# Kernel tuning notes

Hardware: AMD Instinct MI355X
Metric: run time of the kernel (lower is better)

The kernel has to match this reference:

```python
import jax, jax.numpy as jnp
import numpy as np

B, NQ, NK, D = 64, 1024, 1024, 128
MASK_VALUE = -1e6


def setup_inputs() -> dict:
    key = jax.random.key(0)
    kq, kk, kv, kl = jax.random.split(key, 4)
    queries = jax.random.normal(kq, (B, NQ, D), dtype=jnp.float32)
    keys = jax.random.normal(kk, (B, NK, D), dtype=jnp.float32)
    values = jax.random.normal(kv, (B, NK, D), dtype=jnp.float32)
    valid_lens = jax.random.randint(kl, (B,), 1, NK + 1, dtype=jnp.int32)
    return {"queries": queries, "keys": keys, "values": values, "valid_lens": valid_lens}


def reference(queries, keys, values, valid_lens):
    d = queries.shape[-1]
    # scores: [B, Nq, Nk]
    scores = jnp.einsum("bqd,bkd->bqk", queries, keys) / jnp.sqrt(jnp.float32(d))
    # valid_lens [B] -> mask over last (key) axis, same for every query row
    key_pos = jnp.arange(scores.shape[-1])  # [Nk]
    mask = key_pos[None, None, :] < valid_lens[:, None, None]  # [B,1,Nk] broadcast
    scores = jnp.where(mask, scores, jnp.float32(MASK_VALUE))
    attn = jax.nn.softmax(scores, axis=-1)
    # dropout p=0.0 (eval): identity
    return jnp.einsum("bqk,bkd->bqd", attn, values)
```

## Files before the change

### kernel.cpp

```cpp
#include <hip/hip_runtime.h>

typedef __bf16 bf16x8 __attribute__((ext_vector_type(8)));
typedef __bf16 bf16x2 __attribute__((ext_vector_type(2)));
typedef float f32x4 __attribute__((ext_vector_type(4)));
typedef int i32x4 __attribute__((ext_vector_type(4)));

namespace {
constexpr int kNQ = 1024;
constexpr int kNK = 1024;
constexpr int kD = 128;
constexpr int kBK = 32;
constexpr int kTileElems = 4096;
constexpr float kScaleLog2e = 0.12751742f;
}

__device__ __forceinline__ int packbf(float a, float b) {
    bf16x2 t; t[0] = (__bf16)a; t[1] = (__bf16)b;
    return __builtin_bit_cast(int, t);
}

__device__ __forceinline__ void async16(const __bf16* g, const __bf16* l) {
    __builtin_amdgcn_global_load_lds(
        (const __attribute__((address_space(1))) void*)g,
        (__attribute__((address_space(3))) void*)l, 16, 0, 0);
}

__global__ void repack(const float* __restrict__ K, const float* __restrict__ V,
                       const int* __restrict__ VL,
                       __bf16* __restrict__ Kimg, __bf16* __restrict__ Vimg,
                       int* __restrict__ perm) {
    const int blk = blockIdx.x;

    if (blk == 64 * 32) {
        const int t = threadIdx.x;
        if (t < 64) {
            const int v = VL[t];
            int rank = 0;
            for (int j = 0; j < 64; ++j) {
                const int vj = VL[j];
                rank += (vj > v) || (vj == v && j < t);
            }
            perm[rank] = t;
        }
        return;
    }

    const int b = blk >> 5, t = blk & 31;
    if (t * kBK >= VL[b]) return;
    const int tid = threadIdx.x;
    __shared__ float vbuf[32 * 132];

    const size_t tileofs = (size_t)(b * 32 + t) * kTileElems;

    #pragma unroll
    for (int it = 0; it < 2; ++it) {
        const int chunk = tid + it * 256;
        const int k = chunk >> 4;
        const int p = chunk & 15;
        const int c = p ^ (k & 15);
        const float* src = K + (((size_t)b * kNK + t * kBK + k) * kD + c * 8);
        const f32x4 x0 = *(const f32x4*)src;
        const f32x4 x1 = *(const f32x4*)(src + 4);
        bf16x8 h;
        #pragma unroll
        for (int j = 0; j < 4; ++j) { h[j] = (__bf16)x0[j]; h[4 + j] = (__bf16)x1[j]; }
        *(bf16x8*)(Kimg + tileofs + chunk * 8) = h;
    }

    {
        const int r = tid >> 3, col0 = (tid & 7) * 16;
        const float* src = V + (((size_t)b * kNK + t * kBK + r) * kD + col0);
        #pragma unroll
        for (int j = 0; j < 4; ++j) {
            const f32x4 x = *(const f32x4*)(src + j * 4);
            *(f32x4*)&vbuf[r * 132 + col0 + j * 4] = x;
        }
    }
    __syncthreads();
    #pragma unroll
    for (int it = 0; it < 2; ++it) {
        const int chunk = tid + it * 256;
        const int d = chunk >> 2;
        const int p = chunk & 3;
        const int q = p ^ ((d >> 1) & 3);
        bf16x8 h;
        #pragma unroll
        for (int j = 0; j < 8; ++j) h[j] = (__bf16)vbuf[(q * 8 + j) * 132 + d];
        *(bf16x8*)(Vimg + tileofs + chunk * 8) = h;
    }
}

__global__ __launch_bounds__(512, 4)
void fa_fwd(const float* __restrict__ Q, const int* __restrict__ VL,
            const int* __restrict__ perm, const __bf16* __restrict__ Kimg,
            const __bf16* __restrict__ Vimg, float* __restrict__ O)
{
    __shared__ __align__(16) __bf16 kls[4][kTileElems];
    __shared__ __align__(16) __bf16 vls[4][kTileElems];

    const int tid  = threadIdx.x;
    const int wave = tid >> 6;
    const int lane = tid & 63;
    const int quad = lane >> 4;
    const int c16  = lane & 15;

    const int i = blockIdx.x;
    const int j = i & 255;
    const int rank = (i >> 8) ? (511 - j) : j;

    const int b  = perm[rank >> 3];
    const int q0 = (rank & 7) * 128 + wave * 16;

    const int valid  = VL[b];
    const int ntiles = (valid + kBK - 1) / kBK;
    const size_t bT  = (size_t)b * 32;

    auto stage = [&](int slot, int t) {
        const __bf16* kg = Kimg + (bT + t) * kTileElems;
        const __bf16* vg = Vimg + (bT + t) * kTileElems;
        const int seg = wave * 512;
        async16(kg + seg + lane * 8, &kls[slot][seg]);
        async16(vg + seg + lane * 8, &vls[slot][seg]);
    };

    stage(0, 0);
    if (ntiles > 1) stage(1, 1);

    bf16x8 qf[4];
    {
        const float* qp = Q + ((size_t)b * kNQ + q0 + c16) * kD + quad * 8;
        #pragma unroll
        for (int f = 0; f < 4; ++f) {
            const f32x4 x0 = *(const f32x4*)(qp + f * 32);
            const f32x4 x1 = *(const f32x4*)(qp + f * 32 + 4);
            #pragma unroll
            for (int jj = 0; jj < 4; ++jj) {
                qf[f][jj]     = (__bf16)x0[jj];
                qf[f][4 + jj] = (__bf16)x1[jj];
            }
        }
    }

    bf16x8 ones;
    #pragma unroll
    for (int jj = 0; jj < 8; ++jj) ones[jj] = (__bf16)1.0f;

    f32x4 acc[9];
    #pragma unroll
    for (int f = 0; f < 9; ++f) {
        acc[f][0] = 0.f; acc[f][1] = 0.f; acc[f][2] = 0.f; acc[f][3] = 0.f;
    }

    const int a0 = ((quad & 1) << 7) + (c16 << 2);
    const int a1 = a0 + 64;
    const bool lo = quad < 2;

    const int vsw = (quad ^ ((c16 >> 1) & 3)) << 3;

    for (int t = 0; t < ntiles; ++t) {
        if (t + 2 < ntiles) {
            stage((t + 2) & 3, t + 2);
            asm volatile("s_waitcnt vmcnt(4)" ::: "memory");
        } else if (t + 1 < ntiles) {
            asm volatile("s_waitcnt vmcnt(2)" ::: "memory");
        } else {
            asm volatile("s_waitcnt vmcnt(0)" ::: "memory");
        }
        __builtin_amdgcn_s_barrier();
        __builtin_amdgcn_sched_barrier(0);

        const __bf16* kbuf = kls[t & 3];
        const __bf16* vbuf = vls[t & 3];

        f32x4 s0a = {0.f,0.f,0.f,0.f}, s0b = {0.f,0.f,0.f,0.f};
        f32x4 s1a = {0.f,0.f,0.f,0.f}, s1b = {0.f,0.f,0.f,0.f};
        __builtin_amdgcn_s_setprio(1);
        #pragma unroll
        for (int f = 0; f < 2; ++f) {
            const bf16x8 kf = *(const bf16x8*)&kbuf[c16 * 128 + (((f * 4 + quad) ^ c16) << 3)];
            s0a = __builtin_amdgcn_mfma_f32_16x16x32_bf16(kf, qf[f], s0a, 0, 0, 0);
        }
        #pragma unroll
        for (int f = 2; f < 4; ++f) {
            const bf16x8 kf = *(const bf16x8*)&kbuf[c16 * 128 + (((f * 4 + quad) ^ c16) << 3)];
            s0b = __builtin_amdgcn_mfma_f32_16x16x32_bf16(kf, qf[f], s0b, 0, 0, 0);
        }
        #pragma unroll
        for (int f = 0; f < 2; ++f) {
            const bf16x8 kf = *(const bf16x8*)&kbuf[(16 + c16) * 128 + (((f * 4 + quad) ^ c16) << 3)];
            s1a = __builtin_amdgcn_mfma_f32_16x16x32_bf16(kf, qf[f], s1a, 0, 0, 0);
        }
        #pragma unroll
        for (int f = 2; f < 4; ++f) {
            const bf16x8 kf = *(const bf16x8*)&kbuf[(16 + c16) * 128 + (((f * 4 + quad) ^ c16) << 3)];
            s1b = __builtin_amdgcn_mfma_f32_16x16x32_bf16(kf, qf[f], s1b, 0, 0, 0);
        }
        __builtin_amdgcn_s_setprio(0);
        f32x4 s0 = s0a + s0b;
        f32x4 s1 = s1a + s1b;

        const int kb = t * kBK;
        if (kb + kBK > valid) {
            #pragma unroll
            for (int r = 0; r < 4; ++r) {
                if (kb + quad * 4 + r >= valid)      s0[r] = -1e30f;
                if (kb + 16 + quad * 4 + r >= valid) s1[r] = -1e30f;
            }
        }

        #pragma unroll
        for (int r = 0; r < 4; ++r) {
            s0[r] = __builtin_amdgcn_exp2f(s0[r] * kScaleLog2e);
            s1[r] = __builtin_amdgcn_exp2f(s1[r] * kScaleLog2e);
        }

        const int pp01 = packbf(s0[0], s0[1]), pp23 = packbf(s0[2], s0[3]);
        const int qq01 = packbf(s1[0], s1[1]), qq23 = packbf(s1[2], s1[3]);
        const int b0p = __builtin_amdgcn_ds_bpermute(a0, pp01);
        const int b0q = __builtin_amdgcn_ds_bpermute(a0, qq01);
        const int b1p = __builtin_amdgcn_ds_bpermute(a0, pp23);
        const int b1q = __builtin_amdgcn_ds_bpermute(a0, qq23);
        const int b2p = __builtin_amdgcn_ds_bpermute(a1, pp01);
        const int b2q = __builtin_amdgcn_ds_bpermute(a1, qq01);
        const int b3p = __builtin_amdgcn_ds_bpermute(a1, pp23);
        const int b3q = __builtin_amdgcn_ds_bpermute(a1, qq23);
        i32x4 pd;
        pd[0] = lo ? b0p : b0q;
        pd[1] = lo ? b1p : b1q;
        pd[2] = lo ? b2p : b2q;
        pd[3] = lo ? b3p : b3q;
        const bf16x8 pf = __builtin_bit_cast(bf16x8, pd);

        __builtin_amdgcn_s_setprio(1);
        acc[8] = __builtin_amdgcn_mfma_f32_16x16x32_bf16(pf, ones, acc[8], 0, 0, 0);
        #pragma unroll
        for (int f = 0; f < 8; ++f) {
            const bf16x8 vf = *(const bf16x8*)&vbuf[(f * 16 + c16) * 32 + vsw];
            acc[f] = __builtin_amdgcn_mfma_f32_16x16x32_bf16(pf, vf, acc[f], 0, 0, 0);
        }
        __builtin_amdgcn_s_setprio(0);
    }

    float* ob = O + ((size_t)b * kNQ + q0) * kD;
    #pragma unroll
    for (int r = 0; r < 4; ++r) {
        const float inv = 1.0f / acc[8][r];
        #pragma unroll
        for (int f = 0; f < 8; ++f) {
            ob[(quad * 4 + r) * kD + f * 16 + c16] = acc[f][r] * inv;
        }
    }
}

extern "C" void kernel_launch(void* const* d_in, const int* in_sizes, int n_in,
                              void* d_out, int out_size, void* d_ws, size_t ws_size,
                              hipStream_t stream) {
    const float* Q = (const float*)d_in[0];
    const float* K = (const float*)d_in[1];
    const float* V = (const float*)d_in[2];
    const int*  VL = (const int*)d_in[3];
    float* O = (float*)d_out;

    int* perm = (int*)d_ws;
    __bf16* Kimg = (__bf16*)((char*)d_ws + 4096);
    __bf16* Vimg = (__bf16*)((char*)d_ws + 4096 + (size_t)16 * 1024 * 1024);

    repack<<<dim3(64 * 32 + 1), 256, 0, stream>>>(K, V, VL, Kimg, Vimg, perm);
    fa_fwd<<<dim3(512), 512, 0, stream>>>(Q, VL, perm, Kimg, Vimg, O);
}
```

Measured before the change: 164.1 us.

## Process two 16-row query tiles per wave with 256-thread blocks

Each wave now handles 32 query rows as two 16-row sub-tiles that share every K and V fragment read from LDS. This halves the LDS traffic per MFMA and halves the waves per block (256 threads), with each wave issuing twice as many async loads per stage. The cost is more registers per wave (two accumulator sets and two Q fragment sets), with the launch bounds changed to match, and fewer waves available to hide latency.

```diff
diff --git a/kernel.cpp b/kernel.cpp
--- a/kernel.cpp
+++ b/kernel.cpp
@@ -90,7 +90,7 @@
     }
 }
 
-__global__ __launch_bounds__(512, 4)
+__global__ __launch_bounds__(256, 2)
 void fa_fwd(const float* __restrict__ Q, const int* __restrict__ VL,
             const int* __restrict__ perm, const __bf16* __restrict__ Kimg,
             const __bf16* __restrict__ Vimg, float* __restrict__ O)
@@ -109,7 +109,7 @@
     const int rank = (i >> 8) ? (511 - j) : j;
 
     const int b  = perm[rank >> 3];
-    const int q0 = (rank & 7) * 128 + wave * 16;
+    const int q0 = (rank & 7) * 128 + wave * 32;
 
     const int valid  = VL[b];
     const int ntiles = (valid + kBK - 1) / kBK;
@@ -118,25 +118,33 @@
     auto stage = [&](int slot, int t) {
         const __bf16* kg = Kimg + (bT + t) * kTileElems;
         const __bf16* vg = Vimg + (bT + t) * kTileElems;
-        const int seg = wave * 512;
-        async16(kg + seg + lane * 8, &kls[slot][seg]);
-        async16(vg + seg + lane * 8, &vls[slot][seg]);
+        #pragma unroll
+        for (int ii = 0; ii < 2; ++ii) {
+            const int seg = wave * 1024 + ii * 512;
+            async16(kg + seg + lane * 8, &kls[slot][seg]);
+            async16(vg + seg + lane * 8, &vls[slot][seg]);
+        }
     };
 
     stage(0, 0);
     if (ntiles > 1) stage(1, 1);
 
-    bf16x8 qf[4];
+    bf16x8 qfA[4], qfB[4];
     {
-        const float* qp = Q + ((size_t)b * kNQ + q0 + c16) * kD + quad * 8;
+        const float* qpA = Q + ((size_t)b * kNQ + q0 + c16) * kD + quad * 8;
+        const float* qpB = qpA + 16 * kD;
         #pragma unroll
         for (int f = 0; f < 4; ++f) {
-            const f32x4 x0 = *(const f32x4*)(qp + f * 32);
-            const f32x4 x1 = *(const f32x4*)(qp + f * 32 + 4);
+            const f32x4 a0v = *(const f32x4*)(qpA + f * 32);
+            const f32x4 a1v = *(const f32x4*)(qpA + f * 32 + 4);
+            const f32x4 b0v = *(const f32x4*)(qpB + f * 32);
+            const f32x4 b1v = *(const f32x4*)(qpB + f * 32 + 4);
             #pragma unroll
             for (int jj = 0; jj < 4; ++jj) {
-                qf[f][jj]     = (__bf16)x0[jj];
-                qf[f][4 + jj] = (__bf16)x1[jj];
+                qfA[f][jj]     = (__bf16)a0v[jj];
+                qfA[f][4 + jj] = (__bf16)a1v[jj];
+                qfB[f][jj]     = (__bf16)b0v[jj];
+                qfB[f][4 + jj] = (__bf16)b1v[jj];
             }
         }
     }
@@ -145,11 +153,14 @@
     #pragma unroll
     for (int jj = 0; jj < 8; ++jj) ones[jj] = (__bf16)1.0f;
 
-    f32x4 acc[9];
-    #pragma unroll
-    for (int f = 0; f < 9; ++f) {
-        acc[f][0] = 0.f; acc[f][1] = 0.f; acc[f][2] = 0.f; acc[f][3] = 0.f;
-    }
+    f32x4 accA[8], accB[8], lA, lB;
+    #pragma unroll
+    for (int f = 0; f < 8; ++f) {
+        accA[f][0]=0.f; accA[f][1]=0.f; accA[f][2]=0.f; accA[f][3]=0.f;
+        accB[f][0]=0.f; accB[f][1]=0.f; accB[f][2]=0.f; accB[f][3]=0.f;
+    }
+    lA[0]=lA[1]=lA[2]=lA[3]=0.f;
+    lB[0]=lB[1]=lB[2]=lB[3]=0.f;
 
     const int a0 = ((quad & 1) << 7) + (c16 << 2);
     const int a1 = a0 + 64;
@@ -160,9 +171,9 @@
     for (int t = 0; t < ntiles; ++t) {
         if (t + 2 < ntiles) {
             stage((t + 2) & 3, t + 2);
+            asm volatile("s_waitcnt vmcnt(8)" ::: "memory");
+        } else if (t + 1 < ntiles) {
             asm volatile("s_waitcnt vmcnt(4)" ::: "memory");
-        } else if (t + 1 < ntiles) {
-            asm volatile("s_waitcnt vmcnt(2)" ::: "memory");
         } else {
             asm volatile("s_waitcnt vmcnt(0)" ::: "memory");
         }
@@ -172,71 +183,84 @@
         const __bf16* kbuf = kls[t & 3];
         const __bf16* vbuf = vls[t & 3];
 
-        f32x4 s0a = {0.f,0.f,0.f,0.f}, s0b = {0.f,0.f,0.f,0.f};
-        f32x4 s1a = {0.f,0.f,0.f,0.f}, s1b = {0.f,0.f,0.f,0.f};
+        f32x4 sA0 = {0.f,0.f,0.f,0.f}, sA1 = {0.f,0.f,0.f,0.f};
+        f32x4 sB0 = {0.f,0.f,0.f,0.f}, sB1 = {0.f,0.f,0.f,0.f};
         __builtin_amdgcn_s_setprio(1);
         #pragma unroll
-        for (int f = 0; f < 2; ++f) {
-            const bf16x8 kf = *(const bf16x8*)&kbuf[c16 * 128 + (((f * 4 + quad) ^ c16) << 3)];
-            s0a = __builtin_amdgcn_mfma_f32_16x16x32_bf16(kf, qf[f], s0a, 0, 0, 0);
-        }
-        #pragma unroll
-        for (int f = 2; f < 4; ++f) {
-            const bf16x8 kf = *(const bf16x8*)&kbuf[c16 * 128 + (((f * 4 + quad) ^ c16) << 3)];
-            s0b = __builtin_amdgcn_mfma_f32_16x16x32_bf16(kf, qf[f], s0b, 0, 0, 0);
-        }
-        #pragma unroll
-        for (int f = 0; f < 2; ++f) {
-            const bf16x8 kf = *(const bf16x8*)&kbuf[(16 + c16) * 128 + (((f * 4 + quad) ^ c16) << 3)];
-            s1a = __builtin_amdgcn_mfma_f32_16x16x32_bf16(kf, qf[f], s1a, 0, 0, 0);
-        }
-        #pragma unroll
-        for (int f = 2; f < 4; ++f) {
-            const bf16x8 kf = *(const bf16x8*)&kbuf[(16 + c16) * 128 + (((f * 4 + quad) ^ c16) << 3)];
-            s1b = __builtin_amdgcn_mfma_f32_16x16x32_bf16(kf, qf[f], s1b, 0, 0, 0);
+        for (int f = 0; f < 4; ++f) {
+            const int sw = ((f * 4 + quad) ^ c16) << 3;
+            const bf16x8 kf0 = *(const bf16x8*)&kbuf[c16 * 128 + sw];
+            const bf16x8 kf1 = *(const bf16x8*)&kbuf[(16 + c16) * 128 + sw];
+            sA0 = __builtin_amdgcn_mfma_f32_16x16x32_bf16(kf0, qfA[f], sA0, 0, 0, 0);
+            sB0 = __builtin_amdgcn_mfma_f32_16x16x32_bf16(kf0, qfB[f], sB0, 0, 0, 0);
+            sA1 = __builtin_amdgcn_mfma_f32_16x16x32_bf16(kf1, qfA[f], sA1, 0, 0, 0);
+            sB1 = __builtin_amdgcn_mfma_f32_16x16x32_bf16(kf1, qfB[f], sB1, 0, 0, 0);
         }
         __builtin_amdgcn_s_setprio(0);
-        f32x4 s0 = s0a + s0b;
-        f32x4 s1 = s1a + s1b;
 
         const int kb = t * kBK;
         if (kb + kBK > valid) {
             #pragma unroll
             for (int r = 0; r < 4; ++r) {
-                if (kb + quad * 4 + r >= valid)      s0[r] = -1e30f;
-                if (kb + 16 + quad * 4 + r >= valid) s1[r] = -1e30f;
+                if (kb + quad * 4 + r >= valid) { sA0[r] = -1e30f; sB0[r] = -1e30f; }
+                if (kb + 16 + quad * 4 + r >= valid) { sA1[r] = -1e30f; sB1[r] = -1e30f; }
             }
         }
 
         #pragma unroll
         for (int r = 0; r < 4; ++r) {
-            s0[r] = __builtin_amdgcn_exp2f(s0[r] * kScaleLog2e);
-            s1[r] = __builtin_amdgcn_exp2f(s1[r] * kScaleLog2e);
-        }
-
-        const int pp01 = packbf(s0[0], s0[1]), pp23 = packbf(s0[2], s0[3]);
-        const int qq01 = packbf(s1[0], s1[1]), qq23 = packbf(s1[2], s1[3]);
-        const int b0p = __builtin_amdgcn_ds_bpermute(a0, pp01);
-        const int b0q = __builtin_amdgcn_ds_bpermute(a0, qq01);
-        const int b1p = __builtin_amdgcn_ds_bpermute(a0, pp23);
-        const int b1q = __builtin_amdgcn_ds_bpermute(a0, qq23);
-        const int b2p = __builtin_amdgcn_ds_bpermute(a1, pp01);
-        const int b2q = __builtin_amdgcn_ds_bpermute(a1, qq01);
-        const int b3p = __builtin_amdgcn_ds_bpermute(a1, pp23);
-        const int b3q = __builtin_amdgcn_ds_bpermute(a1, qq23);
-        i32x4 pd;
-        pd[0] = lo ? b0p : b0q;
-        pd[1] = lo ? b1p : b1q;
-        pd[2] = lo ? b2p : b2q;
-        pd[3] = lo ? b3p : b3q;
-        const bf16x8 pf = __builtin_bit_cast(bf16x8, pd);
+            sA0[r] = __builtin_amdgcn_exp2f(sA0[r] * kScaleLog2e);
+            sA1[r] = __builtin_amdgcn_exp2f(sA1[r] * kScaleLog2e);
+            sB0[r] = __builtin_amdgcn_exp2f(sB0[r] * kScaleLog2e);
+            sB1[r] = __builtin_amdgcn_exp2f(sB1[r] * kScaleLog2e);
+        }
+
+        bf16x8 pfA, pfB;
+        {
+            const int pp01 = packbf(sA0[0], sA0[1]), pp23 = packbf(sA0[2], sA0[3]);
+            const int qq01 = packbf(sA1[0], sA1[1]), qq23 = packbf(sA1[2], sA1[3]);
+            const int b0p = __builtin_amdgcn_ds_bpermute(a0, pp01);
+            const int b0q = __builtin_amdgcn_ds_bpermute(a0, qq01);
+            const int b1p = __builtin_amdgcn_ds_bpermute(a0, pp23);
+            const int b1q = __builtin_amdgcn_ds_bpermute(a0, qq23);
+            const int b2p = __builtin_amdgcn_ds_bpermute(a1, pp01);
+            const int b2q = __builtin_amdgcn_ds_bpermute(a1, qq01);
+            const int b3p = __builtin_amdgcn_ds_bpermute(a1, pp23);
+            const int b3q = __builtin_amdgcn_ds_bpermute(a1, qq23);
+            i32x4 pd;
+            pd[0] = lo ? b0p : b0q;
+            pd[1] = lo ? b1p : b1q;
+            pd[2] = lo ? b2p : b2q;
+            pd[3] = lo ? b3p : b3q;
+            pfA = __builtin_bit_cast(bf16x8, pd);
+        }
+        {
+            const int pp01 = packbf(sB0[0], sB0[1]), pp23 = packbf(sB0[2], sB0[3]);
+            const int qq01 = packbf(sB1[0], sB1[1]), qq23 = packbf(sB1[2], sB1[3]);
+            const int b0p = __builtin_amdgcn_ds_bpermute(a0, pp01);
+            const int b0q = __builtin_amdgcn_ds_bpermute(a0, qq01);
+            const int b1p = __builtin_amdgcn_ds_bpermute(a0, pp23);
+            const int b1q = __builtin_amdgcn_ds_bpermute(a0, qq23);
+            const int b2p = __builtin_amdgcn_ds_bpermute(a1, pp01);
+            const int b2q = __builtin_amdgcn_ds_bpermute(a1, qq01);
+            const int b3p = __builtin_amdgcn_ds_bpermute(a1, pp23);
+            const int b3q = __builtin_amdgcn_ds_bpermute(a1, qq23);
+            i32x4 pd;
+            pd[0] = lo ? b0p : b0q;
+            pd[1] = lo ? b1p : b1q;
+            pd[2] = lo ? b2p : b2q;
+            pd[3] = lo ? b3p : b3q;
+            pfB = __builtin_bit_cast(bf16x8, pd);
+        }
 
         __builtin_amdgcn_s_setprio(1);
-        acc[8] = __builtin_amdgcn_mfma_f32_16x16x32_bf16(pf, ones, acc[8], 0, 0, 0);
+        lA = __builtin_amdgcn_mfma_f32_16x16x32_bf16(pfA, ones, lA, 0, 0, 0);
+        lB = __builtin_amdgcn_mfma_f32_16x16x32_bf16(pfB, ones, lB, 0, 0, 0);
         #pragma unroll
         for (int f = 0; f < 8; ++f) {
             const bf16x8 vf = *(const bf16x8*)&vbuf[(f * 16 + c16) * 32 + vsw];
-            acc[f] = __builtin_amdgcn_mfma_f32_16x16x32_bf16(pf, vf, acc[f], 0, 0, 0);
+            accA[f] = __builtin_amdgcn_mfma_f32_16x16x32_bf16(pfA, vf, accA[f], 0, 0, 0);
+            accB[f] = __builtin_amdgcn_mfma_f32_16x16x32_bf16(pfB, vf, accB[f], 0, 0, 0);
         }
         __builtin_amdgcn_s_setprio(0);
     }
@@ -244,10 +268,12 @@
     float* ob = O + ((size_t)b * kNQ + q0) * kD;
     #pragma unroll
     for (int r = 0; r < 4; ++r) {
-        const float inv = 1.0f / acc[8][r];
+        const float invA = 1.0f / lA[r];
+        const float invB = 1.0f / lB[r];
         #pragma unroll
         for (int f = 0; f < 8; ++f) {
-            ob[(quad * 4 + r) * kD + f * 16 + c16] = acc[f][r] * inv;
+            ob[(quad * 4 + r) * kD + f * 16 + c16]        = accA[f][r] * invA;
+            ob[(16 + quad * 4 + r) * kD + f * 16 + c16]   = accB[f][r] * invB;
         }
     }
 }
@@ -266,5 +292,5 @@
     __bf16* Vimg = (__bf16*)((char*)d_ws + 4096 + (size_t)16 * 1024 * 1024);
 
     repack<<<dim3(64 * 32 + 1), 256, 0, stream>>>(K, V, VL, Kimg, Vimg, perm);
-    fa_fwd<<<dim3(512), 512, 0, stream>>>(Q, VL, perm, Kimg, Vimg, O);
-}
+    fa_fwd<<<dim3(512), 256, 0, stream>>>(Q, VL, perm, Kimg, Vimg, O);
+}
```

After: 167.9 us. 2.3% more time.

## Process two K/V tiles per loop iteration with a single barrier

Applied to the files above, without the earlier changes.

Restructures the attention main loop so each iteration waits for all outstanding loads, issues one barrier, prefetches the next two tiles, and then runs both QK^T products before both softmax/PV phases. The aim is to halve barrier and wait overhead and to give the scheduler two independent MFMA chains to interleave. The cost is a full vmcnt(0) wait in place of the finer-grained partial waits, which may expose more load latency, plus higher register pressure from holding two tiles of scores at once.

```diff
diff --git a/kernel.cpp b/kernel.cpp
--- a/kernel.cpp
+++ b/kernel.cpp
@@ -157,21 +157,7 @@
 
     const int vsw = (quad ^ ((c16 >> 1) & 3)) << 3;
 
-    for (int t = 0; t < ntiles; ++t) {
-        if (t + 2 < ntiles) {
-            stage((t + 2) & 3, t + 2);
-            asm volatile("s_waitcnt vmcnt(4)" ::: "memory");
-        } else if (t + 1 < ntiles) {
-            asm volatile("s_waitcnt vmcnt(2)" ::: "memory");
-        } else {
-            asm volatile("s_waitcnt vmcnt(0)" ::: "memory");
-        }
-        __builtin_amdgcn_s_barrier();
-        __builtin_amdgcn_sched_barrier(0);
-
-        const __bf16* kbuf = kls[t & 3];
-        const __bf16* vbuf = vls[t & 3];
-
+    auto qk = [&](const __bf16* kbuf, f32x4& s0, f32x4& s1) {
         f32x4 s0a = {0.f,0.f,0.f,0.f}, s0b = {0.f,0.f,0.f,0.f};
         f32x4 s1a = {0.f,0.f,0.f,0.f}, s1b = {0.f,0.f,0.f,0.f};
         __builtin_amdgcn_s_setprio(1);
@@ -196,10 +182,11 @@
             s1b = __builtin_amdgcn_mfma_f32_16x16x32_bf16(kf, qf[f], s1b, 0, 0, 0);
         }
         __builtin_amdgcn_s_setprio(0);
-        f32x4 s0 = s0a + s0b;
-        f32x4 s1 = s1a + s1b;
-
-        const int kb = t * kBK;
+        s0 = s0a + s0b;
+        s1 = s1a + s1b;
+    };
+
+    auto smpv = [&](f32x4 s0, f32x4 s1, const __bf16* vbuf, int kb) {
         if (kb + kBK > valid) {
             #pragma unroll
             for (int r = 0; r < 4; ++r) {
@@ -207,13 +194,11 @@
                 if (kb + 16 + quad * 4 + r >= valid) s1[r] = -1e30f;
             }
         }
-
         #pragma unroll
         for (int r = 0; r < 4; ++r) {
             s0[r] = __builtin_amdgcn_exp2f(s0[r] * kScaleLog2e);
             s1[r] = __builtin_amdgcn_exp2f(s1[r] * kScaleLog2e);
         }
-
         const int pp01 = packbf(s0[0], s0[1]), pp23 = packbf(s0[2], s0[3]);
         const int qq01 = packbf(s1[0], s1[1]), qq23 = packbf(s1[2], s1[3]);
         const int b0p = __builtin_amdgcn_ds_bpermute(a0, pp01);
@@ -239,6 +224,31 @@
             acc[f] = __builtin_amdgcn_mfma_f32_16x16x32_bf16(pf, vf, acc[f], 0, 0, 0);
         }
         __builtin_amdgcn_s_setprio(0);
+    };
+
+    int t = 0;
+    while (t + 1 < ntiles) {
+        asm volatile("s_waitcnt vmcnt(0)" ::: "memory");
+        __builtin_amdgcn_s_barrier();
+        __builtin_amdgcn_sched_barrier(0);
+
+        if (t + 2 < ntiles) stage((t + 2) & 3, t + 2);
+        if (t + 3 < ntiles) stage((t + 3) & 3, t + 3);
+
+        f32x4 s0_0, s1_0, s0_1, s1_1;
+        qk(kls[t & 3], s0_0, s1_0);
+        qk(kls[(t + 1) & 3], s0_1, s1_1);
+        smpv(s0_0, s1_0, vls[t & 3], t * kBK);
+        smpv(s0_1, s1_1, vls[(t + 1) & 3], (t + 1) * kBK);
+        t += 2;
+    }
+    if (t < ntiles) {
+        asm volatile("s_waitcnt vmcnt(0)" ::: "memory");
+        __builtin_amdgcn_s_barrier();
+        __builtin_amdgcn_sched_barrier(0);
+        f32x4 s0_0, s1_0;
+        qk(kls[t & 3], s0_0, s1_0);
+        smpv(s0_0, s1_0, vls[t & 3], t * kBK);
     }
 
     float* ob = O + ((size_t)b * kNQ + q0) * kD;
```

After: 164.4 us. About the same (+0.1%).

## Switch attention kernel to 32x32x16 MFMA with 4 waves of 32 query rows

Applied to the files above, without the earlier changes.

Rewrites the flash-attention inner loop to use 32x32x16 bf16 MFMA instead of 16x16x32. Each wave now handles 32 query rows and the block shrinks to 256 threads. The row-sum is accumulated on the VALU instead of through an extra MFMA against a ones vector. The P operand is rearranged with a cross-half bpermute exchange, and the staging loop issues twice as many async loads per wave. The aim is to raise MFMA efficiency and cut the LDS reads of K and V per query row, at the cost of larger accumulator register footprint and fewer waves per block.

```diff
diff --git a/kernel.cpp b/kernel.cpp
--- a/kernel.cpp
+++ b/kernel.cpp
@@ -3,6 +3,7 @@
 typedef __bf16 bf16x8 __attribute__((ext_vector_type(8)));
 typedef __bf16 bf16x2 __attribute__((ext_vector_type(2)));
 typedef float f32x4 __attribute__((ext_vector_type(4)));
+typedef float f32x16 __attribute__((ext_vector_type(16)));
 typedef int i32x4 __attribute__((ext_vector_type(4)));
 
 namespace {
@@ -90,7 +91,7 @@
     }
 }
 
-__global__ __launch_bounds__(512, 4)
+__global__ __launch_bounds__(256, 2)
 void fa_fwd(const float* __restrict__ Q, const int* __restrict__ VL,
             const int* __restrict__ perm, const __bf16* __restrict__ Kimg,
             const __bf16* __restrict__ Vimg, float* __restrict__ O)
@@ -101,15 +102,15 @@
     const int tid  = threadIdx.x;
     const int wave = tid >> 6;
     const int lane = tid & 63;
-    const int quad = lane >> 4;
-    const int c16  = lane & 15;
+    const int key  = lane & 31;
+    const int hi   = lane >> 5;
 
     const int i = blockIdx.x;
     const int j = i & 255;
     const int rank = (i >> 8) ? (511 - j) : j;
 
     const int b  = perm[rank >> 3];
-    const int q0 = (rank & 7) * 128 + wave * 16;
+    const int q0 = (rank & 7) * 128 + wave * 32;
 
     const int valid  = VL[b];
     const int ntiles = (valid + kBK - 1) / kBK;
@@ -118,51 +119,48 @@
     auto stage = [&](int slot, int t) {
         const __bf16* kg = Kimg + (bT + t) * kTileElems;
         const __bf16* vg = Vimg + (bT + t) * kTileElems;
-        const int seg = wave * 512;
-        async16(kg + seg + lane * 8, &kls[slot][seg]);
-        async16(vg + seg + lane * 8, &vls[slot][seg]);
+        #pragma unroll
+        for (int ii = 0; ii < 2; ++ii) {
+            const int seg = wave * 1024 + ii * 512;
+            async16(kg + seg + lane * 8, &kls[slot][seg]);
+            async16(vg + seg + lane * 8, &vls[slot][seg]);
+        }
     };
 
     stage(0, 0);
     if (ntiles > 1) stage(1, 1);
 
-    bf16x8 qf[4];
+    bf16x8 qf[8];
     {
-        const float* qp = Q + ((size_t)b * kNQ + q0 + c16) * kD + quad * 8;
-        #pragma unroll
-        for (int f = 0; f < 4; ++f) {
-            const f32x4 x0 = *(const f32x4*)(qp + f * 32);
-            const f32x4 x1 = *(const f32x4*)(qp + f * 32 + 4);
+        const float* qp = Q + ((size_t)b * kNQ + q0 + key) * kD + hi * 8;
+        #pragma unroll
+        for (int s = 0; s < 8; ++s) {
+            const f32x4 x0 = *(const f32x4*)(qp + s * 16);
+            const f32x4 x1 = *(const f32x4*)(qp + s * 16 + 4);
             #pragma unroll
             for (int jj = 0; jj < 4; ++jj) {
-                qf[f][jj]     = (__bf16)x0[jj];
-                qf[f][4 + jj] = (__bf16)x1[jj];
+                qf[s][jj]     = (__bf16)x0[jj];
+                qf[s][4 + jj] = (__bf16)x1[jj];
             }
         }
     }
 
-    bf16x8 ones;
-    #pragma unroll
-    for (int jj = 0; jj < 8; ++jj) ones[jj] = (__bf16)1.0f;
-
-    f32x4 acc[9];
-    #pragma unroll
-    for (int f = 0; f < 9; ++f) {
-        acc[f][0] = 0.f; acc[f][1] = 0.f; acc[f][2] = 0.f; acc[f][3] = 0.f;
-    }
-
-    const int a0 = ((quad & 1) << 7) + (c16 << 2);
-    const int a1 = a0 + 64;
-    const bool lo = quad < 2;
-
-    const int vsw = (quad ^ ((c16 >> 1) & 3)) << 3;
+    f32x16 acc0, acc1, acc2, acc3;
+    #pragma unroll
+    for (int r = 0; r < 16; ++r) { acc0[r]=0.f; acc1[r]=0.f; acc2[r]=0.f; acc3[r]=0.f; }
+    float lsum = 0.f;
+
+    const int kterm = key & 15;
+    const int vterm = (key >> 1) & 3;
+    const int xaddr = (lane ^ 32) << 2;
+    const int hi4   = hi << 2;
 
     for (int t = 0; t < ntiles; ++t) {
         if (t + 2 < ntiles) {
             stage((t + 2) & 3, t + 2);
+            asm volatile("s_waitcnt vmcnt(8)" ::: "memory");
+        } else if (t + 1 < ntiles) {
             asm volatile("s_waitcnt vmcnt(4)" ::: "memory");
-        } else if (t + 1 < ntiles) {
-            asm volatile("s_waitcnt vmcnt(2)" ::: "memory");
         } else {
             asm volatile("s_waitcnt vmcnt(0)" ::: "memory");
         }
@@ -172,83 +170,98 @@
         const __bf16* kbuf = kls[t & 3];
         const __bf16* vbuf = vls[t & 3];
 
-        f32x4 s0a = {0.f,0.f,0.f,0.f}, s0b = {0.f,0.f,0.f,0.f};
-        f32x4 s1a = {0.f,0.f,0.f,0.f}, s1b = {0.f,0.f,0.f,0.f};
+        f32x16 sa, sb;
+        #pragma unroll
+        for (int r = 0; r < 16; ++r) { sa[r] = 0.f; sb[r] = 0.f; }
         __builtin_amdgcn_s_setprio(1);
         #pragma unroll
-        for (int f = 0; f < 2; ++f) {
-            const bf16x8 kf = *(const bf16x8*)&kbuf[c16 * 128 + (((f * 4 + quad) ^ c16) << 3)];
-            s0a = __builtin_amdgcn_mfma_f32_16x16x32_bf16(kf, qf[f], s0a, 0, 0, 0);
-        }
-        #pragma unroll
-        for (int f = 2; f < 4; ++f) {
-            const bf16x8 kf = *(const bf16x8*)&kbuf[c16 * 128 + (((f * 4 + quad) ^ c16) << 3)];
-            s0b = __builtin_amdgcn_mfma_f32_16x16x32_bf16(kf, qf[f], s0b, 0, 0, 0);
-        }
-        #pragma unroll
-        for (int f = 0; f < 2; ++f) {
-            const bf16x8 kf = *(const bf16x8*)&kbuf[(16 + c16) * 128 + (((f * 4 + quad) ^ c16) << 3)];
-            s1a = __builtin_amdgcn_mfma_f32_16x16x32_bf16(kf, qf[f], s1a, 0, 0, 0);
-        }
-        #pragma unroll
-        for (int f = 2; f < 4; ++f) {
-            const bf16x8 kf = *(const bf16x8*)&kbuf[(16 + c16) * 128 + (((f * 4 + quad) ^ c16) << 3)];
-            s1b = __builtin_amdgcn_mfma_f32_16x16x32_bf16(kf, qf[f], s1b, 0, 0, 0);
+        for (int s = 0; s < 4; ++s) {
+            const bf16x8 kf = *(const bf16x8*)&kbuf[key * 128 + (((s * 2 + hi) ^ kterm) << 3)];
+            sa = __builtin_amdgcn_mfma_f32_32x32x16_bf16(kf, qf[s], sa, 0, 0, 0);
+        }
+        #pragma unroll
+        for (int s = 4; s < 8; ++s) {
+            const bf16x8 kf = *(const bf16x8*)&kbuf[key * 128 + (((s * 2 + hi) ^ kterm) << 3)];
+            sb = __builtin_amdgcn_mfma_f32_32x32x16_bf16(kf, qf[s], sb, 0, 0, 0);
         }
         __builtin_amdgcn_s_setprio(0);
-        f32x4 s0 = s0a + s0b;
-        f32x4 s1 = s1a + s1b;
+        f32x16 sv = sa + sb;
 
         const int kb = t * kBK;
         if (kb + kBK > valid) {
             #pragma unroll
-            for (int r = 0; r < 4; ++r) {
-                if (kb + quad * 4 + r >= valid)      s0[r] = -1e30f;
-                if (kb + 16 + quad * 4 + r >= valid) s1[r] = -1e30f;
+            for (int r = 0; r < 16; ++r) {
+                const int cr = (r & 3) + 8 * (r >> 2);
+                if (kb + cr + hi4 >= valid) sv[r] = -1e30f;
             }
         }
 
         #pragma unroll
-        for (int r = 0; r < 4; ++r) {
-            s0[r] = __builtin_amdgcn_exp2f(s0[r] * kScaleLog2e);
-            s1[r] = __builtin_amdgcn_exp2f(s1[r] * kScaleLog2e);
-        }
-
-        const int pp01 = packbf(s0[0], s0[1]), pp23 = packbf(s0[2], s0[3]);
-        const int qq01 = packbf(s1[0], s1[1]), qq23 = packbf(s1[2], s1[3]);
-        const int b0p = __builtin_amdgcn_ds_bpermute(a0, pp01);
-        const int b0q = __builtin_amdgcn_ds_bpermute(a0, qq01);
-        const int b1p = __builtin_amdgcn_ds_bpermute(a0, pp23);
-        const int b1q = __builtin_amdgcn_ds_bpermute(a0, qq23);
-        const int b2p = __builtin_amdgcn_ds_bpermute(a1, pp01);
-        const int b2q = __builtin_amdgcn_ds_bpermute(a1, qq01);
-        const int b3p = __builtin_amdgcn_ds_bpermute(a1, pp23);
-        const int b3q = __builtin_amdgcn_ds_bpermute(a1, qq23);
-        i32x4 pd;
-        pd[0] = lo ? b0p : b0q;
-        pd[1] = lo ? b1p : b1q;
-        pd[2] = lo ? b2p : b2q;
-        pd[3] = lo ? b3p : b3q;
-        const bf16x8 pf = __builtin_bit_cast(bf16x8, pd);
+        for (int r = 0; r < 16; ++r) sv[r] = __builtin_amdgcn_exp2f(sv[r] * kScaleLog2e);
+
+        {
+            float a0 = sv[0]+sv[1], a1 = sv[2]+sv[3], a2 = sv[4]+sv[5], a3 = sv[6]+sv[7];
+            float a4 = sv[8]+sv[9], a5 = sv[10]+sv[11], a6 = sv[12]+sv[13], a7 = sv[14]+sv[15];
+            lsum += ((a0+a1)+(a2+a3)) + ((a4+a5)+(a6+a7));
+        }
+
+        int w[8], pw[8];
+        #pragma unroll
+        for (int jp = 0; jp < 8; ++jp) w[jp] = packbf(sv[2*jp], sv[2*jp+1]);
+        #pragma unroll
+        for (int jp = 0; jp < 8; ++jp) pw[jp] = __builtin_amdgcn_ds_bpermute(xaddr, w[jp]);
+
+        i32x4 f0, f1;
+        f0[0] = hi ? pw[2] : w[0];
+        f0[1] = hi ? pw[3] : w[1];
+        f0[2] = hi ? w[2]  : pw[0];
+        f0[3] = hi ? w[3]  : pw[1];
+        f1[0] = hi ? pw[6] : w[4];
+        f1[1] = hi ? pw[7] : w[5];
+        f1[2] = hi ? w[6]  : pw[4];
+        f1[3] = hi ? w[7]  : pw[5];
+        const bf16x8 pfs0 = __builtin_bit_cast(bf16x8, f0);
+        const bf16x8 pfs1 = __builtin_bit_cast(bf16x8, f1);
 
         __builtin_amdgcn_s_setprio(1);
-        acc[8] = __builtin_amdgcn_mfma_f32_16x16x32_bf16(pf, ones, acc[8], 0, 0, 0);
-        #pragma unroll
-        for (int f = 0; f < 8; ++f) {
-            const bf16x8 vf = *(const bf16x8*)&vbuf[(f * 16 + c16) * 32 + vsw];
-            acc[f] = __builtin_amdgcn_mfma_f32_16x16x32_bf16(pf, vf, acc[f], 0, 0, 0);
+        {
+            const int vb0 = key * 32 + (((0 + hi) ^ vterm) << 3);
+            const int vb1 = key * 32 + (((2 + hi) ^ vterm) << 3);
+            const bf16x8 v00 = *(const bf16x8*)&vbuf[0 * 1024 + vb0];
+            const bf16x8 v10 = *(const bf16x8*)&vbuf[1 * 1024 + vb0];
+            const bf16x8 v20 = *(const bf16x8*)&vbuf[2 * 1024 + vb0];
+            const bf16x8 v30 = *(const bf16x8*)&vbuf[3 * 1024 + vb0];
+            acc0 = __builtin_amdgcn_mfma_f32_32x32x16_bf16(pfs0, v00, acc0, 0, 0, 0);
+            acc1 = __builtin_amdgcn_mfma_f32_32x32x16_bf16(pfs0, v10, acc1, 0, 0, 0);
+            acc2 = __builtin_amdgcn_mfma_f32_32x32x16_bf16(pfs0, v20, acc2, 0, 0, 0);
+            acc3 = __builtin_amdgcn_mfma_f32_32x32x16_bf16(pfs0, v30, acc3, 0, 0, 0);
+            const bf16x8 v01 = *(const bf16x8*)&vbuf[0 * 1024 + vb1];
+            const bf16x8 v11 = *(const bf16x8*)&vbuf[1 * 1024 + vb1];
+            const bf16x8 v21 = *(const bf16x8*)&vbuf[2 * 1024 + vb1];
+            const bf16x8 v31 = *(const bf16x8*)&vbuf[3 * 1024 + vb1];
+            acc0 = __builtin_amdgcn_mfma_f32_32x32x16_bf16(pfs1, v01, acc0, 0, 0, 0);
+            acc1 = __builtin_amdgcn_mfma_f32_32x32x16_bf16(pfs1, v11, acc1, 0, 0, 0);
+            acc2 = __builtin_amdgcn_mfma_f32_32x32x16_bf16(pfs1, v21, acc2, 0, 0, 0);
+            acc3 = __builtin_amdgcn_mfma_f32_32x32x16_bf16(pfs1, v31, acc3, 0, 0, 0);
         }
         __builtin_amdgcn_s_setprio(0);
     }
 
+    const int plb = __builtin_amdgcn_ds_bpermute(xaddr, __builtin_bit_cast(int, lsum));
+    const float linv = 1.0f / (lsum + __builtin_bit_cast(float, plb));
     float* ob = O + ((size_t)b * kNQ + q0) * kD;
-    #pragma unroll
-    for (int r = 0; r < 4; ++r) {
-        const float inv = 1.0f / acc[8][r];
-        #pragma unroll
-        for (int f = 0; f < 8; ++f) {
-            ob[(quad * 4 + r) * kD + f * 16 + c16] = acc[f][r] * inv;
-        }
+    const int hib = hi << 4;
+    #pragma unroll
+    for (int r = 0; r < 16; ++r) {
+        const int cr = (r & 3) + 8 * (r >> 2);
+        const int iv = __builtin_amdgcn_ds_bpermute((cr << 2) + hib,
+                                                    __builtin_bit_cast(int, linv));
+        const float inv = __builtin_bit_cast(float, iv);
+        const int q = cr + hi4;
+        ob[q * kD +   0 + key] = acc0[r] * inv;
+        ob[q * kD +  32 + key] = acc1[r] * inv;
+        ob[q * kD +  64 + key] = acc2[r] * inv;
+        ob[q * kD +  96 + key] = acc3[r] * inv;
     }
 }
 
@@ -266,5 +279,5 @@
     __bf16* Vimg = (__bf16*)((char*)d_ws + 4096 + (size_t)16 * 1024 * 1024);
 
     repack<<<dim3(64 * 32 + 1), 256, 0, stream>>>(K, V, VL, Kimg, Vimg, perm);
-    fa_fwd<<<dim3(512), 512, 0, stream>>>(Q, VL, perm, Kimg, Vimg, O);
-}
+    fa_fwd<<<dim3(512), 256, 0, stream>>>(Q, VL, perm, Kimg, Vimg, O);
+}
```

Measured after the change: 169.2 us. 3.1% more time.
